# Kernel optimization log

Measured on AMD Instinct MI355X. Metric: run time of the kernel, lower is better.

Reference implementation:

```python
import jax, jax.numpy as jnp
import numpy as np

F_IN, HID, F_OUT = 8, 64, 8
R, C = 256, 4096
NUM_SETS, N_IND, M = 3, 4096, 4096


def setup_inputs() -> dict:
    key = jax.random.key(0)
    k0, k1, k2 = jax.random.split(key, 3)
    input_tensor = jax.random.normal(k0, (F_IN, R, C), dtype=jnp.float32)
    w1 = jax.random.normal(k1, (HID, 3 * F_IN), dtype=jnp.float32) * 0.1
    b1 = jnp.zeros((HID,), jnp.float32)
    w2 = jax.random.normal(k2, (F_OUT, HID), dtype=jnp.float32) * 0.1
    b2 = jnp.zeros((F_OUT,), jnp.float32)
    rng = np.random.default_rng(0)
    def make_ind():
        # col0: permutation of [0, N_IND) (duplicate-free scatter-set destinations)
        # col1: random source column in [0, C)
        col0 = np.stack([rng.permutation(N_IND) for _ in range(NUM_SETS)])
        col1 = rng.integers(0, C, size=(NUM_SETS, N_IND))
        return jnp.asarray(np.stack([col0, col1], axis=-1), jnp.int32)
    ind0, ind1, ind2 = make_ind(), make_ind(), make_ind()
    mix_ind = jnp.asarray(rng.integers(0, N_IND, size=(NUM_SETS, 3, M)), jnp.int32)
    return {"input_tensor": input_tensor, "w1": w1, "b1": b1, "w2": w2, "b2": b2,
            "ind0": ind0, "ind1": ind1, "ind2": ind2, "mix_ind": mix_ind}


def reference(input_tensor, w1, b1, w2, b2, ind0, ind1, ind2, mix_ind):
    # Output for row r depends only on input row r, so we process all R at once
    # (the original chunk loop over R is pure tiling).
    F_in, Rr, Cc = input_tensor.shape
    F_out = w2.shape[0]
    num_sets = ind0.shape[0]

    def project(ind, mi):
        # res[..., ind[:,0]] = input[..., ind[:,1]]; then take slots mi -> [F_in, R, M]
        n = ind.shape[0]
        res = jnp.zeros((F_in, Rr, n), input_tensor.dtype)
        res = res.at[..., ind[:, 0]].set(input_tensor[..., ind[:, 1]])
        return res[..., mi]

    out_rcf = jnp.zeros((Rr, Cc, F_out), input_tensor.dtype)  # zeros = include_self baseline
    for s in range(num_sets):
        c1 = project(ind0[s], mix_ind[s, 0])
        c2 = project(ind1[s], mix_ind[s, 1])
        c3 = project(ind2[s], mix_ind[s, 2])
        c = jnp.concatenate([c1, c2, c3], axis=0)          # [3F_in, R, M]
        c_flat = c.transpose(1, 2, 0).reshape(-1, 3 * F_in)  # [R*M, 3F_in]
        a1 = jax.nn.relu(c_flat @ w1.T + b1)                 # [R*M, HID]
        d = (a1 @ w2.T + b2).reshape(Rr, -1, F_out)          # [R, M, F_out]
        for i, ind in enumerate((ind0[s], ind1[s], ind2[s])):
            idx = ind[:, 1][mix_ind[s, i]]                   # [M] target columns in C
            out_rcf = out_rcf.at[:, idx, :].max(d)           # amax scatter, include_self
    return out_rcf.transpose(2, 0, 1)                        # [F_out, R, C]
```

## Files before the change

kernel.cpp:

```cpp
#include <hip/hip_runtime.h>
#include <cstdint>

#define F_IN   8
#define HID    64
#define F_OUTD 8
#define RDIM   256
#define CDIM   4096
#define NSETS  3
#define NIND   4096
#define MDIM   4096
#define MAXL   64
#define GC     16
#define MPW    4

using short8 = __attribute__((ext_vector_type(8))) short;
using f32x4  = __attribute__((ext_vector_type(4))) float;

__device__ inline unsigned int cvtpk(float a, float b) {
    unsigned int r;
    asm("v_cvt_pk_bf16_f32 %0, %1, %2" : "=v"(r) : "v"(a), "v"(b));
    return r;
}
__device__ inline unsigned int pkmaxu(unsigned int a, unsigned int b) {
    unsigned int r;
    asm("v_pk_max_u16 %0, %1, %2" : "=v"(r) : "v"(a), "v"(b));
    return r;
}

__global__ __launch_bounds__(256)
void prep_in(const float* __restrict__ in, unsigned short* __restrict__ out) {
    const int PADH = 264;
    __shared__ unsigned short tile[32 * PADH];
    int c0 = blockIdx.x * 32, r0 = blockIdx.y * 32;
    int t = threadIdx.x;
    int tx = t & 31, ty = t >> 5;
#pragma unroll
    for (int f = 0; f < 8; f += 2)
#pragma unroll
        for (int rr = 0; rr < 4; rr++) {
            int r = ty + rr * 8;
            float v0 = in[((size_t)f * RDIM + (r0 + r)) * CDIM + c0 + tx];
            float v1 = in[((size_t)(f + 1) * RDIM + (r0 + r)) * CDIM + c0 + tx];
            *(unsigned int*)&tile[tx * PADH + r * 8 + f] = cvtpk(v0, v1);
        }
    __syncthreads();
    int r = t & 31, cl = t >> 5;
#pragma unroll
    for (int cc = 0; cc < 4; cc++) {
        int c = cc * 8 + cl;
        uint4 v = *(const uint4*)&tile[c * PADH + r * 8];
        *(uint4*)(out + (((size_t)(c0 + c) * RDIM) + (r0 + r)) * 8) = v;
    }
}

__global__ void build_inv(const int* __restrict__ ind0, const int* __restrict__ ind1,
                          const int* __restrict__ ind2,
                          const float* __restrict__ w1, const float* __restrict__ w2,
                          int* __restrict__ inv, int* __restrict__ mergecnt,
                          unsigned short* __restrict__ w1bf, unsigned short* __restrict__ w2bf) {
    int k  = blockIdx.x * 256 + threadIdx.x;
    int si = blockIdx.y;
    int s_ = si / 3, i_ = si % 3;
    const int* ind = (i_ == 0 ? ind0 : (i_ == 1 ? ind1 : ind2)) + (size_t)s_ * NIND * 2;
    int c0 = ind[2 * k];
    inv[(size_t)si * NIND + c0] = k;
    if (si == 0) mergecnt[k] = 0;
    if (blockIdx.x == 0 && blockIdx.y == 0) {
        int t = threadIdx.x;
        for (int i = t; i < 64 * 32; i += 256) {
            int j = i >> 5, kk = i & 31;
            w1bf[i] = (kk < 24) ? (unsigned short)(cvtpk(w1[j * 24 + kk], 0.f) & 0xffff) : 0;
        }
        for (int i = t; i < 16 * 64; i += 256) {
            int f = i >> 6, kg = i & 63;
            int hi = kg >> 5, q = (kg >> 3) & 3, e = kg & 7;
            int j = (hi << 5) + ((e >> 2) << 4) + (q << 2) + (e & 3);
            w2bf[i] = (f < 8) ? (unsigned short)(cvtpk(w2[f * 64 + j], 0.f) & 0xffff) : 0;
        }
    }
}

__global__ void build_buckets(const int* __restrict__ ind0, const int* __restrict__ ind1,
                              const int* __restrict__ ind2, const int* __restrict__ mix,
                              int* __restrict__ mergecnt, int* __restrict__ mergelist) {
    int m  = blockIdx.x * 256 + threadIdx.x;
    int si = blockIdx.y;
    int s_ = si / 3, i_ = si % 3;
    const int* ind = (i_ == 0 ? ind0 : (i_ == 1 ? ind1 : ind2)) + (size_t)s_ * NIND * 2;
    int mi = mix[(size_t)si * MDIM + m];
    int c  = ind[2 * mi + 1];
    int slot = atomicAdd(&mergecnt[c], 1);
    if (slot < MAXL) mergelist[(size_t)c * MAXL + slot] = s_ * MDIM + m;
}

__global__ __launch_bounds__(256, 2)
void mlp_store(const unsigned short* __restrict__ inT2,
               const unsigned short* __restrict__ w1bf,
               const unsigned short* __restrict__ w2bf,
               const float* __restrict__ b1, const float* __restrict__ b2,
               const int* __restrict__ ind0, const int* __restrict__ ind1,
               const int* __restrict__ ind2, const int* __restrict__ mix,
               const int* __restrict__ inv,
               unsigned short* __restrict__ dbuf) {
    int t    = threadIdx.x;
    int wave = t >> 6, lane = t & 63;
    int lo = lane & 15, q = lane >> 4;

    int wid  = blockIdx.x * 4 + wave;
    int mgrp = wid & 1023;
    int half = (wid >> 10) & 1;
    int s_   = wid >> 11;
    int m0   = mgrp * MPW;

    short8 A1[4], A2[2];
#pragma unroll
    for (int tt = 0; tt < 4; tt++)
        A1[tt] = *(const short8*)(w1bf + ((16 * tt + lo) << 5) + (q << 3));
#pragma unroll
    for (int kk = 0; kk < 2; kk++)
        A2[kk] = *(const short8*)(w2bf + (lo << 6) + (kk << 5) + (q << 3));

    f32x4 bbv[4];
#pragma unroll
    for (int tt = 0; tt < 4; tt++)
#pragma unroll
        for (int rg = 0; rg < 4; rg++)
            bbv[tt][rg] = b1[16 * tt + 4 * q + rg];
    f32x4 b2f;
#pragma unroll
    for (int rg = 0; rg < 4; rg++) {
        int f = 4 * q + rg;
        b2f[rg] = (f < 8) ? b2[f] : 0.f;
    }

    int gq[MPW] = {0, 0, 0, 0};
    if (q < 3) {
        int si = s_ * 3 + q;
        const int* indq = (q == 0 ? ind0 : (q == 1 ? ind1 : ind2)) + (size_t)s_ * NIND * 2;
        int mi[MPW], kk[MPW];
#pragma unroll
        for (int u = 0; u < MPW; u++) mi[u] = mix[(size_t)si * MDIM + m0 + u];
#pragma unroll
        for (int u = 0; u < MPW; u++) kk[u] = inv[(size_t)si * NIND + mi[u]];
#pragma unroll
        for (int u = 0; u < MPW; u++) gq[u] = indq[2 * kk[u] + 1];
    }
    const unsigned short* srcs[MPW];
#pragma unroll
    for (int u = 0; u < MPW; u++)
        srcs[u] = inT2 + ((size_t)gq[u] * RDIM + half * 128 + lo) * 8;

    unsigned short* dst = dbuf + (size_t)(s_ * MDIM + m0) * 2048 + half * 1024 + lo * 8 + q * 4;

    union U { unsigned int u[4]; short8 s; };
    const short8 zero8 = {0, 0, 0, 0, 0, 0, 0, 0};

    short8 Bcur = zero8;
    if (q < 3) Bcur = *(const short8*)srcs[0];
#pragma unroll
    for (int it = 0; it < MPW * 8; it++) {
        const int u = it >> 3, j = it & 7;
        short8 Bnext = Bcur;
        if (it < MPW * 8 - 1 && q < 3)
            Bnext = *(const short8*)(srcs[(it + 1) >> 3] + ((it + 1) & 7) * 128);

        f32x4 a0 = __builtin_amdgcn_mfma_f32_16x16x32_bf16(A1[0], Bcur, bbv[0], 0, 0, 0);
        f32x4 a1 = __builtin_amdgcn_mfma_f32_16x16x32_bf16(A1[1], Bcur, bbv[1], 0, 0, 0);
        f32x4 a2 = __builtin_amdgcn_mfma_f32_16x16x32_bf16(A1[2], Bcur, bbv[2], 0, 0, 0);
        f32x4 a3 = __builtin_amdgcn_mfma_f32_16x16x32_bf16(A1[3], Bcur, bbv[3], 0, 0, 0);

        U ba, bb;
        ba.u[0] = cvtpk(fmaxf(a0[0], 0.f), fmaxf(a0[1], 0.f));
        ba.u[1] = cvtpk(fmaxf(a0[2], 0.f), fmaxf(a0[3], 0.f));
        ba.u[2] = cvtpk(fmaxf(a1[0], 0.f), fmaxf(a1[1], 0.f));
        ba.u[3] = cvtpk(fmaxf(a1[2], 0.f), fmaxf(a1[3], 0.f));
        bb.u[0] = cvtpk(fmaxf(a2[0], 0.f), fmaxf(a2[1], 0.f));
        bb.u[1] = cvtpk(fmaxf(a2[2], 0.f), fmaxf(a2[3], 0.f));
        bb.u[2] = cvtpk(fmaxf(a3[0], 0.f), fmaxf(a3[1], 0.f));
        bb.u[3] = cvtpk(fmaxf(a3[2], 0.f), fmaxf(a3[3], 0.f));

        f32x4 o = __builtin_amdgcn_mfma_f32_16x16x32_bf16(A2[0], ba.s, b2f, 0, 0, 0);
        o = __builtin_amdgcn_mfma_f32_16x16x32_bf16(A2[1], bb.s, o, 0, 0, 0);

        if (q < 2) {
            uint2 ov;
            ov.x = cvtpk(fmaxf(o[0], 0.f), fmaxf(o[1], 0.f));
            ov.y = cvtpk(fmaxf(o[2], 0.f), fmaxf(o[3], 0.f));
            *(uint2*)(dst + (size_t)u * 2048 + j * 128) = ov;
        }
        Bcur = Bnext;
    }
}

__global__ __launch_bounds__(1024)
void gather_max_t(const unsigned short* __restrict__ dbuf, const int* __restrict__ mergecnt,
                  const int* __restrict__ mergelist, float* __restrict__ out) {
    __shared__ unsigned int ldsP[4][64][20];
    __shared__ int mlist[GC][MAXL];
    int t = threadIdx.x;
    int w = t >> 6, lane = t & 63;
    int c0 = blockIdx.x * GC;
    int c  = c0 + w;

    mlist[w][lane] = 0;
    int n = mergecnt[c];
    n = n < 0 ? 0 : (n > MAXL ? MAXL : n);
    if (lane < n) {
        int idx = mergelist[(size_t)c * MAXL + lane];
        idx = idx < 0 ? 0 : (idx >= NSETS * MDIM ? NSETS * MDIM - 1 : idx);
        mlist[w][lane] = idx;
    }
    __syncthreads();

    int r = blockIdx.y * 64 + lane;
    uint4 acc = make_uint4(0u, 0u, 0u, 0u);
    if (n > 0) {
        uint4 p = *(const uint4*)(dbuf + ((size_t)mlist[w][0] * RDIM + r) * 8);
        for (int e = 1; e < n; e++) {
            uint4 nx = *(const uint4*)(dbuf + ((size_t)mlist[w][e] * RDIM + r) * 8);
            acc.x = pkmaxu(acc.x, p.x); acc.y = pkmaxu(acc.y, p.y);
            acc.z = pkmaxu(acc.z, p.z); acc.w = pkmaxu(acc.w, p.w);
            p = nx;
        }
        acc.x = pkmaxu(acc.x, p.x); acc.y = pkmaxu(acc.y, p.y);
        acc.z = pkmaxu(acc.z, p.z); acc.w = pkmaxu(acc.w, p.w);
    }

    ldsP[0][lane][w] = acc.x;
    ldsP[1][lane][w] = acc.y;
    ldsP[2][lane][w] = acc.z;
    ldsP[3][lane][w] = acc.w;
    __syncthreads();

    int f2 = t >> 8, rl = (t >> 2) & 63, cq = t & 3;
    uint4 v = *(const uint4*)&ldsP[f2][rl][cq * 4];
    float4 lo, hi;
    lo.x = fmaxf(__uint_as_float(v.x << 16), 0.f);
    hi.x = fmaxf(__uint_as_float(v.x & 0xffff0000u), 0.f);
    lo.y = fmaxf(__uint_as_float(v.y << 16), 0.f);
    hi.y = fmaxf(__uint_as_float(v.y & 0xffff0000u), 0.f);
    lo.z = fmaxf(__uint_as_float(v.z << 16), 0.f);
    hi.z = fmaxf(__uint_as_float(v.z & 0xffff0000u), 0.f);
    lo.w = fmaxf(__uint_as_float(v.w << 16), 0.f);
    hi.w = fmaxf(__uint_as_float(v.w & 0xffff0000u), 0.f);
    size_t rowoff = (size_t)blockIdx.y * 64 + rl;
    *(float4*)&out[((size_t)(2 * f2) * RDIM + rowoff) * CDIM + c0 + cq * 4] = lo;
    *(float4*)&out[((size_t)(2 * f2 + 1) * RDIM + rowoff) * CDIM + c0 + cq * 4] = hi;
}

extern "C" void kernel_launch(void* const* d_in, const int* in_sizes, int n_in,
                              void* d_out, int out_size, void* d_ws, size_t ws_size,
                              hipStream_t stream) {
    const float* input = (const float*)d_in[0];
    const float* w1    = (const float*)d_in[1];
    const float* b1    = (const float*)d_in[2];
    const float* w2    = (const float*)d_in[3];
    const float* b2    = (const float*)d_in[4];
    const int*   ind0  = (const int*)d_in[5];
    const int*   ind1  = (const int*)d_in[6];
    const int*   ind2  = (const int*)d_in[7];
    const int*   mix   = (const int*)d_in[8];

    const size_t MiB = 1ull << 20;
    char* ws = (char*)d_ws;
    unsigned short* inT2 = (unsigned short*)ws;
    unsigned short* dbuf = (unsigned short*)(ws + 16 * MiB);
    char* tail = ws + 64 * MiB;
    int* inv       = (int*)tail;
    int* mergecnt  = (int*)(tail + 147456);
    int* mergelist = (int*)(tail + 147456 + 16384);
    unsigned short* w1bf = (unsigned short*)(tail + 147456 + 16384 + (size_t)CDIM * MAXL * 4);
    unsigned short* w2bf = w1bf + 64 * 32;

    prep_in<<<dim3(CDIM / 32, RDIM / 32), 256, 0, stream>>>(input, inT2);
    build_inv<<<dim3(NIND / 256, 9), 256, 0, stream>>>(ind0, ind1, ind2, w1, w2,
                                                       inv, mergecnt, w1bf, w2bf);
    build_buckets<<<dim3(MDIM / 256, 9), 256, 0, stream>>>(ind0, ind1, ind2, mix,
                                                           mergecnt, mergelist);
    mlp_store<<<NSETS * 2 * (MDIM / MPW) / 4, 256, 0, stream>>>(inT2, w1bf, w2bf, b1, b2,
                                                                ind0, ind1, ind2, mix, inv, dbuf);
    gather_max_t<<<dim3(CDIM / GC, 4), 1024, 0, stream>>>(dbuf, mergecnt, mergelist,
                                                          (float*)d_out);
}
```

Before: 88.31 us.

## Fuse MLP and gather-max into one kernel, removing the intermediate dbuf

Replaces the two-pass design, where the MLP writes bf16 results for every (set, m) to a large buffer and a second kernel gathers and max-reduces per column, with one fused kernel. Each wave owns a column, walks its bucket list, recomputes the MLP for each contributing entry and max-accumulates in registers. A small precomputed gather table (build_gtab) resolves the three source columns per entry. This removes the round trip through the large intermediate buffer, but work now depends on bucket length, so load is uneven across waves.

Result: slower. 239.8 us (+171.5%).

```diff
diff --git a/kernel.cpp b/kernel.cpp
--- a/kernel.cpp
+++ b/kernel.cpp
@@ -11,7 +11,6 @@
 #define MDIM   4096
 #define MAXL   64
 #define GC     16
-#define MPW    4
 
 using short8 = __attribute__((ext_vector_type(8))) short;
 using f32x4  = __attribute__((ext_vector_type(4))) float;
@@ -93,24 +92,38 @@
     if (slot < MAXL) mergelist[(size_t)c * MAXL + slot] = s_ * MDIM + m;
 }
 
-__global__ __launch_bounds__(256, 2)
-void mlp_store(const unsigned short* __restrict__ inT2,
-               const unsigned short* __restrict__ w1bf,
-               const unsigned short* __restrict__ w2bf,
-               const float* __restrict__ b1, const float* __restrict__ b2,
-               const int* __restrict__ ind0, const int* __restrict__ ind1,
-               const int* __restrict__ ind2, const int* __restrict__ mix,
-               const int* __restrict__ inv,
-               unsigned short* __restrict__ dbuf) {
-    int t    = threadIdx.x;
-    int wave = t >> 6, lane = t & 63;
+__global__ void build_gtab(const int* __restrict__ ind0, const int* __restrict__ ind1,
+                           const int* __restrict__ ind2, const int* __restrict__ mix,
+                           const int* __restrict__ inv, int4* __restrict__ gtab) {
+    int sm = blockIdx.x * 256 + threadIdx.x;
+    int s  = sm >> 12, m = sm & 4095;
+    int g[3];
+#pragma unroll
+    for (int i = 0; i < 3; i++) {
+        int si = s * 3 + i;
+        int mi = mix[(size_t)si * MDIM + m];
+        int k  = inv[(size_t)si * NIND + mi];
+        const int* ind = (i == 0 ? ind0 : (i == 1 ? ind1 : ind2)) + (size_t)s * NIND * 2;
+        g[i] = ind[2 * k + 1];
+    }
+    gtab[sm] = make_int4(g[0], g[1], g[2], 0);
+}
+
+__global__ __launch_bounds__(1024)
+void fused_mlp_gather(const unsigned short* __restrict__ inT2,
+                      const unsigned short* __restrict__ w1bf,
+                      const unsigned short* __restrict__ w2bf,
+                      const float* __restrict__ b1, const float* __restrict__ b2,
+                      const int* __restrict__ mergecnt, const int* __restrict__ mergelist,
+                      const int4* __restrict__ gtab, float* __restrict__ out) {
+    __shared__ unsigned int ldsP[4][16][20];
+    __shared__ int glist[GC][MAXL][4];
+    int t = threadIdx.x;
+    int w = t >> 6, lane = t & 63;
     int lo = lane & 15, q = lane >> 4;
-
-    int wid  = blockIdx.x * 4 + wave;
-    int mgrp = wid & 1023;
-    int half = (wid >> 10) & 1;
-    int s_   = wid >> 11;
-    int m0   = mgrp * MPW;
+    int c0 = blockIdx.x * GC;
+    int c  = c0 + w;
+    int r16 = blockIdx.y * 16;
 
     short8 A1[4], A2[2];
 #pragma unroll
@@ -119,7 +132,6 @@
 #pragma unroll
     for (int kk = 0; kk < 2; kk++)
         A2[kk] = *(const short8*)(w2bf + (lo << 6) + (kk << 5) + (q << 3));
-
     f32x4 bbv[4];
 #pragma unroll
     for (int tt = 0; tt < 4; tt++)
@@ -132,37 +144,38 @@
         int f = 4 * q + rg;
         b2f[rg] = (f < 8) ? b2[f] : 0.f;
     }
-
-    int gq[MPW] = {0, 0, 0, 0};
-    if (q < 3) {
-        int si = s_ * 3 + q;
-        const int* indq = (q == 0 ? ind0 : (q == 1 ? ind1 : ind2)) + (size_t)s_ * NIND * 2;
-        int mi[MPW], kk[MPW];
-#pragma unroll
-        for (int u = 0; u < MPW; u++) mi[u] = mix[(size_t)si * MDIM + m0 + u];
-#pragma unroll
-        for (int u = 0; u < MPW; u++) kk[u] = inv[(size_t)si * NIND + mi[u]];
-#pragma unroll
-        for (int u = 0; u < MPW; u++) gq[u] = indq[2 * kk[u] + 1];
-    }
-    const unsigned short* srcs[MPW];
-#pragma unroll
-    for (int u = 0; u < MPW; u++)
-        srcs[u] = inT2 + ((size_t)gq[u] * RDIM + half * 128 + lo) * 8;
-
-    unsigned short* dst = dbuf + (size_t)(s_ * MDIM + m0) * 2048 + half * 1024 + lo * 8 + q * 4;
+#pragma unroll
+    for (int tt = 0; tt < 4; tt++) asm volatile("" : "+v"(A1[tt]));
+    asm volatile("" : "+v"(A2[0]), "+v"(A2[1]));
+
+    int n = mergecnt[c];
+    n = n < 0 ? 0 : (n > MAXL ? MAXL : n);
+    if (lane < n) {
+        int sm = mergelist[(size_t)c * MAXL + lane];
+        sm = sm < 0 ? 0 : (sm >= NSETS * MDIM ? NSETS * MDIM - 1 : sm);
+        *(int4*)&glist[w][lane][0] = gtab[sm];
+    }
+    __syncthreads();
+
+    const unsigned short* zsrc = w2bf + 512 + lo * 8;
 
     union U { unsigned int u[4]; short8 s; };
     const short8 zero8 = {0, 0, 0, 0, 0, 0, 0, 0};
+    uint2 acc; acc.x = 0u; acc.y = 0u;
 
     short8 Bcur = zero8;
-    if (q < 3) Bcur = *(const short8*)srcs[0];
-#pragma unroll
-    for (int it = 0; it < MPW * 8; it++) {
-        const int u = it >> 3, j = it & 7;
-        short8 Bnext = Bcur;
-        if (it < MPW * 8 - 1 && q < 3)
-            Bnext = *(const short8*)(srcs[(it + 1) >> 3] + ((it + 1) & 7) * 128);
+    if (n > 0) {
+        int g = glist[w][0][q & 3];
+        const unsigned short* p = (q < 3) ? inT2 + ((size_t)g * RDIM + r16 + lo) * 8 : zsrc;
+        Bcur = *(const short8*)p;
+    }
+    for (int e = 0; e < n; e++) {
+        short8 Bnext = zero8;
+        if (e + 1 < n) {
+            int g = glist[w][e + 1][q & 3];
+            const unsigned short* p = (q < 3) ? inT2 + ((size_t)g * RDIM + r16 + lo) * 8 : zsrc;
+            Bnext = *(const short8*)p;
+        }
 
         f32x4 a0 = __builtin_amdgcn_mfma_f32_16x16x32_bf16(A1[0], Bcur, bbv[0], 0, 0, 0);
         f32x4 a1 = __builtin_amdgcn_mfma_f32_16x16x32_bf16(A1[1], Bcur, bbv[1], 0, 0, 0);
@@ -182,70 +195,37 @@
         f32x4 o = __builtin_amdgcn_mfma_f32_16x16x32_bf16(A2[0], ba.s, b2f, 0, 0, 0);
         o = __builtin_amdgcn_mfma_f32_16x16x32_bf16(A2[1], bb.s, o, 0, 0, 0);
 
-        if (q < 2) {
-            uint2 ov;
-            ov.x = cvtpk(fmaxf(o[0], 0.f), fmaxf(o[1], 0.f));
-            ov.y = cvtpk(fmaxf(o[2], 0.f), fmaxf(o[3], 0.f));
-            *(uint2*)(dst + (size_t)u * 2048 + j * 128) = ov;
-        }
+        unsigned int ox = cvtpk(fmaxf(o[0], 0.f), fmaxf(o[1], 0.f));
+        unsigned int oy = cvtpk(fmaxf(o[2], 0.f), fmaxf(o[3], 0.f));
+        acc.x = pkmaxu(acc.x, ox);
+        acc.y = pkmaxu(acc.y, oy);
+
         Bcur = Bnext;
     }
-}
-
-__global__ __launch_bounds__(1024)
-void gather_max_t(const unsigned short* __restrict__ dbuf, const int* __restrict__ mergecnt,
-                  const int* __restrict__ mergelist, float* __restrict__ out) {
-    __shared__ unsigned int ldsP[4][64][20];
-    __shared__ int mlist[GC][MAXL];
-    int t = threadIdx.x;
-    int w = t >> 6, lane = t & 63;
-    int c0 = blockIdx.x * GC;
-    int c  = c0 + w;
-
-    mlist[w][lane] = 0;
-    int n = mergecnt[c];
-    n = n < 0 ? 0 : (n > MAXL ? MAXL : n);
-    if (lane < n) {
-        int idx = mergelist[(size_t)c * MAXL + lane];
-        idx = idx < 0 ? 0 : (idx >= NSETS * MDIM ? NSETS * MDIM - 1 : idx);
-        mlist[w][lane] = idx;
+
+    if (q < 2) {
+        ldsP[2 * q][lo][w]     = acc.x;
+        ldsP[2 * q + 1][lo][w] = acc.y;
     }
     __syncthreads();
 
-    int r = blockIdx.y * 64 + lane;
-    uint4 acc = make_uint4(0u, 0u, 0u, 0u);
-    if (n > 0) {
-        uint4 p = *(const uint4*)(dbuf + ((size_t)mlist[w][0] * RDIM + r) * 8);
-        for (int e = 1; e < n; e++) {
-            uint4 nx = *(const uint4*)(dbuf + ((size_t)mlist[w][e] * RDIM + r) * 8);
-            acc.x = pkmaxu(acc.x, p.x); acc.y = pkmaxu(acc.y, p.y);
-            acc.z = pkmaxu(acc.z, p.z); acc.w = pkmaxu(acc.w, p.w);
-            p = nx;
-        }
-        acc.x = pkmaxu(acc.x, p.x); acc.y = pkmaxu(acc.y, p.y);
-        acc.z = pkmaxu(acc.z, p.z); acc.w = pkmaxu(acc.w, p.w);
-    }
-
-    ldsP[0][lane][w] = acc.x;
-    ldsP[1][lane][w] = acc.y;
-    ldsP[2][lane][w] = acc.z;
-    ldsP[3][lane][w] = acc.w;
-    __syncthreads();
-
-    int f2 = t >> 8, rl = (t >> 2) & 63, cq = t & 3;
-    uint4 v = *(const uint4*)&ldsP[f2][rl][cq * 4];
-    float4 lo, hi;
-    lo.x = fmaxf(__uint_as_float(v.x << 16), 0.f);
-    hi.x = fmaxf(__uint_as_float(v.x & 0xffff0000u), 0.f);
-    lo.y = fmaxf(__uint_as_float(v.y << 16), 0.f);
-    hi.y = fmaxf(__uint_as_float(v.y & 0xffff0000u), 0.f);
-    lo.z = fmaxf(__uint_as_float(v.z << 16), 0.f);
-    hi.z = fmaxf(__uint_as_float(v.z & 0xffff0000u), 0.f);
-    lo.w = fmaxf(__uint_as_float(v.w << 16), 0.f);
-    hi.w = fmaxf(__uint_as_float(v.w & 0xffff0000u), 0.f);
-    size_t rowoff = (size_t)blockIdx.y * 64 + rl;
-    *(float4*)&out[((size_t)(2 * f2) * RDIM + rowoff) * CDIM + c0 + cq * 4] = lo;
-    *(float4*)&out[((size_t)(2 * f2 + 1) * RDIM + rowoff) * CDIM + c0 + cq * 4] = hi;
+    if (t < 512) {
+        int f = t >> 6, rl = (t >> 2) & 15, cq = t & 3;
+        uint4 v = *(const uint4*)&ldsP[f >> 1][rl][cq * 4];
+        float4 ov;
+        if (f & 1) {
+            ov.x = fmaxf(__uint_as_float(v.x & 0xffff0000u), 0.f);
+            ov.y = fmaxf(__uint_as_float(v.y & 0xffff0000u), 0.f);
+            ov.z = fmaxf(__uint_as_float(v.z & 0xffff0000u), 0.f);
+            ov.w = fmaxf(__uint_as_float(v.w & 0xffff0000u), 0.f);
+        } else {
+            ov.x = fmaxf(__uint_as_float(v.x << 16), 0.f);
+            ov.y = fmaxf(__uint_as_float(v.y << 16), 0.f);
+            ov.z = fmaxf(__uint_as_float(v.z << 16), 0.f);
+            ov.w = fmaxf(__uint_as_float(v.w << 16), 0.f);
+        }
+        *(float4*)&out[((size_t)f * RDIM + r16 + rl) * CDIM + c0 + cq * 4] = ov;
+    }
 }
 
 extern "C" void kernel_launch(void* const* d_in, const int* in_sizes, int n_in,
@@ -264,12 +244,12 @@
     const size_t MiB = 1ull << 20;
     char* ws = (char*)d_ws;
     unsigned short* inT2 = (unsigned short*)ws;
-    unsigned short* dbuf = (unsigned short*)(ws + 16 * MiB);
-    char* tail = ws + 64 * MiB;
-    int* inv       = (int*)tail;
-    int* mergecnt  = (int*)(tail + 147456);
-    int* mergelist = (int*)(tail + 147456 + 16384);
-    unsigned short* w1bf = (unsigned short*)(tail + 147456 + 16384 + (size_t)CDIM * MAXL * 4);
+    char* tail = ws + 16 * MiB;
+    int*  inv       = (int*)tail;
+    int*  mergecnt  = (int*)(tail + 147456);
+    int*  mergelist = (int*)(tail + 147456 + 16384);
+    int4* gtab      = (int4*)(tail + 147456 + 16384 + (size_t)CDIM * MAXL * 4);
+    unsigned short* w1bf = (unsigned short*)((char*)gtab + (size_t)NSETS * MDIM * 16);
     unsigned short* w2bf = w1bf + 64 * 32;
 
     prep_in<<<dim3(CDIM / 32, RDIM / 32), 256, 0, stream>>>(input, inT2);
@@ -277,8 +257,7 @@
                                                        inv, mergecnt, w1bf, w2bf);
     build_buckets<<<dim3(MDIM / 256, 9), 256, 0, stream>>>(ind0, ind1, ind2, mix,
                                                            mergecnt, mergelist);
-    mlp_store<<<NSETS * 2 * (MDIM / MPW) / 4, 256, 0, stream>>>(inT2, w1bf, w2bf, b1, b2,
-                                                                ind0, ind1, ind2, mix, inv, dbuf);
-    gather_max_t<<<dim3(CDIM / GC, 4), 1024, 0, stream>>>(dbuf, mergecnt, mergelist,
-                                                          (float*)d_out);
-}
+    build_gtab<<<NSETS * MDIM / 256, 256, 0, stream>>>(ind0, ind1, ind2, mix, inv, gtab);
+    fused_mlp_gather<<<dim3(CDIM / GC, 16), 1024, 0, stream>>>(
+        inT2, w1bf, w2bf, b1, b2, mergecnt, mergelist, gtab, (float*)d_out);
+}
```

## Process two row tiles per gather block and pin MLP weights in registers

Applied to the files above, without the earlier changes.

The gather-max kernel now handles 128 rows per block instead of 64, with two accumulators, and the grid's y dimension is halved. This reuses each loaded merge list for twice the rows and doubles the independent loads in flight. Empty asm barriers in the MLP kernel keep the weight and bias fragments in VGPRs, and the redundant zeroing of mlist is removed. The cost is fewer blocks, an extra LDS round with a second sync, and higher register pressure.

After: 86.08 us. 2.5% less time.

```diff
diff --git a/kernel.cpp b/kernel.cpp
--- a/kernel.cpp
+++ b/kernel.cpp
@@ -133,6 +133,13 @@
         b2f[rg] = (f < 8) ? b2[f] : 0.f;
     }
 
+#pragma unroll
+    for (int tt = 0; tt < 4; tt++) asm volatile("" : "+v"(A1[tt]));
+    asm volatile("" : "+v"(A2[0]), "+v"(A2[1]));
+#pragma unroll
+    for (int tt = 0; tt < 4; tt++) asm volatile("" : "+v"(bbv[tt]));
+    asm volatile("" : "+v"(b2f));
+
     int gq[MPW] = {0, 0, 0, 0};
     if (q < 3) {
         int si = s_ * 3 + q;
@@ -202,7 +209,6 @@
     int c0 = blockIdx.x * GC;
     int c  = c0 + w;
 
-    mlist[w][lane] = 0;
     int n = mergecnt[c];
     n = n < 0 ? 0 : (n > MAXL ? MAXL : n);
     if (lane < n) {
@@ -212,40 +218,54 @@
     }
     __syncthreads();
 
-    int r = blockIdx.y * 64 + lane;
-    uint4 acc = make_uint4(0u, 0u, 0u, 0u);
+    int rbase = blockIdx.y * 128 + lane;
+    uint4 accA = make_uint4(0u, 0u, 0u, 0u);
+    uint4 accB = make_uint4(0u, 0u, 0u, 0u);
     if (n > 0) {
-        uint4 p = *(const uint4*)(dbuf + ((size_t)mlist[w][0] * RDIM + r) * 8);
+        const unsigned short* bp = dbuf + ((size_t)mlist[w][0] * RDIM + rbase) * 8;
+        uint4 pa = *(const uint4*)(bp);
+        uint4 pb = *(const uint4*)(bp + 64 * 8);
         for (int e = 1; e < n; e++) {
-            uint4 nx = *(const uint4*)(dbuf + ((size_t)mlist[w][e] * RDIM + r) * 8);
-            acc.x = pkmaxu(acc.x, p.x); acc.y = pkmaxu(acc.y, p.y);
-            acc.z = pkmaxu(acc.z, p.z); acc.w = pkmaxu(acc.w, p.w);
-            p = nx;
-        }
-        acc.x = pkmaxu(acc.x, p.x); acc.y = pkmaxu(acc.y, p.y);
-        acc.z = pkmaxu(acc.z, p.z); acc.w = pkmaxu(acc.w, p.w);
-    }
-
-    ldsP[0][lane][w] = acc.x;
-    ldsP[1][lane][w] = acc.y;
-    ldsP[2][lane][w] = acc.z;
-    ldsP[3][lane][w] = acc.w;
-    __syncthreads();
-
-    int f2 = t >> 8, rl = (t >> 2) & 63, cq = t & 3;
-    uint4 v = *(const uint4*)&ldsP[f2][rl][cq * 4];
-    float4 lo, hi;
-    lo.x = fmaxf(__uint_as_float(v.x << 16), 0.f);
-    hi.x = fmaxf(__uint_as_float(v.x & 0xffff0000u), 0.f);
-    lo.y = fmaxf(__uint_as_float(v.y << 16), 0.f);
-    hi.y = fmaxf(__uint_as_float(v.y & 0xffff0000u), 0.f);
-    lo.z = fmaxf(__uint_as_float(v.z << 16), 0.f);
-    hi.z = fmaxf(__uint_as_float(v.z & 0xffff0000u), 0.f);
-    lo.w = fmaxf(__uint_as_float(v.w << 16), 0.f);
-    hi.w = fmaxf(__uint_as_float(v.w & 0xffff0000u), 0.f);
-    size_t rowoff = (size_t)blockIdx.y * 64 + rl;
-    *(float4*)&out[((size_t)(2 * f2) * RDIM + rowoff) * CDIM + c0 + cq * 4] = lo;
-    *(float4*)&out[((size_t)(2 * f2 + 1) * RDIM + rowoff) * CDIM + c0 + cq * 4] = hi;
+            const unsigned short* bq = dbuf + ((size_t)mlist[w][e] * RDIM + rbase) * 8;
+            uint4 qa = *(const uint4*)(bq);
+            uint4 qb = *(const uint4*)(bq + 64 * 8);
+            accA.x = pkmaxu(accA.x, pa.x); accA.y = pkmaxu(accA.y, pa.y);
+            accA.z = pkmaxu(accA.z, pa.z); accA.w = pkmaxu(accA.w, pa.w);
+            accB.x = pkmaxu(accB.x, pb.x); accB.y = pkmaxu(accB.y, pb.y);
+            accB.z = pkmaxu(accB.z, pb.z); accB.w = pkmaxu(accB.w, pb.w);
+            pa = qa; pb = qb;
+        }
+        accA.x = pkmaxu(accA.x, pa.x); accA.y = pkmaxu(accA.y, pa.y);
+        accA.z = pkmaxu(accA.z, pa.z); accA.w = pkmaxu(accA.w, pa.w);
+        accB.x = pkmaxu(accB.x, pb.x); accB.y = pkmaxu(accB.y, pb.y);
+        accB.z = pkmaxu(accB.z, pb.z); accB.w = pkmaxu(accB.w, pb.w);
+    }
+
+#pragma unroll
+    for (int p = 0; p < 2; p++) {
+        if (p) __syncthreads();
+        uint4 a = p ? accB : accA;
+        ldsP[0][lane][w] = a.x;
+        ldsP[1][lane][w] = a.y;
+        ldsP[2][lane][w] = a.z;
+        ldsP[3][lane][w] = a.w;
+        __syncthreads();
+
+        int f2 = t >> 8, rl = (t >> 2) & 63, cq = t & 3;
+        uint4 v = *(const uint4*)&ldsP[f2][rl][cq * 4];
+        float4 lo, hi;
+        lo.x = fmaxf(__uint_as_float(v.x << 16), 0.f);
+        hi.x = fmaxf(__uint_as_float(v.x & 0xffff0000u), 0.f);
+        lo.y = fmaxf(__uint_as_float(v.y << 16), 0.f);
+        hi.y = fmaxf(__uint_as_float(v.y & 0xffff0000u), 0.f);
+        lo.z = fmaxf(__uint_as_float(v.z << 16), 0.f);
+        hi.z = fmaxf(__uint_as_float(v.z & 0xffff0000u), 0.f);
+        lo.w = fmaxf(__uint_as_float(v.w << 16), 0.f);
+        hi.w = fmaxf(__uint_as_float(v.w & 0xffff0000u), 0.f);
+        size_t rowoff = (size_t)blockIdx.y * 128 + p * 64 + rl;
+        *(float4*)&out[((size_t)(2 * f2) * RDIM + rowoff) * CDIM + c0 + cq * 4] = lo;
+        *(float4*)&out[((size_t)(2 * f2 + 1) * RDIM + rowoff) * CDIM + c0 + cq * 4] = hi;
+    }
 }
 
 extern "C" void kernel_launch(void* const* d_in, const int* in_sizes, int n_in,
@@ -279,6 +299,6 @@
                                                            mergecnt, mergelist);
     mlp_store<<<NSETS * 2 * (MDIM / MPW) / 4, 256, 0, stream>>>(inT2, w1bf, w2bf, b1, b2,
                                                                 ind0, ind1, ind2, mix, inv, dbuf);
-    gather_max_t<<<dim3(CDIM / GC, 4), 1024, 0, stream>>>(dbuf, mergecnt, mergelist,
+    gather_max_t<<<dim3(CDIM / GC, 2), 1024, 0, stream>>>(dbuf, mergecnt, mergelist,
                                                           (float*)d_out);
 }
```
